# Performance work log

Hardware: AMD Instinct MI355X
Metric: run time of the kernel (lower is better)

Reference implementation:

```python
import jax, jax.numpy as jnp
import numpy as np

UFEAT_DIM = 256
MAPFEAT_DIM = 64


def setup_inputs() -> dict:
    key = jax.random.key(0)
    k1, k2, k3, k4 = jax.random.split(key, 4)
    ufeat = jax.random.normal(k1, (32, 512, UFEAT_DIM), dtype=jnp.float32)
    mapfeat = jax.random.normal(k2, (32, 4096, MAPFEAT_DIM), dtype=jnp.float32)
    # weight_norm(Linear, dim=None): W = g * V / ||V||_F, g scalar
    v_w = jax.random.normal(k3, (MAPFEAT_DIM, UFEAT_DIM), dtype=jnp.float32) * 0.05
    g = jnp.asarray(1.0, dtype=jnp.float32)
    b = jax.random.normal(k4, (MAPFEAT_DIM,), dtype=jnp.float32) * 0.05
    return {"ufeat": ufeat, "mapfeat": mapfeat, "v_w": v_w, "g": g, "b": b}


def reference(ufeat, mapfeat, v_w, g, b):
    # weight-normalized linear (dim=None -> scalar g over Frobenius norm)
    w = g * v_w / jnp.linalg.norm(v_w)
    proj = jax.nn.relu(jnp.einsum("bud,md->bum", ufeat, w) + b)  # [B, U, M]
    norm = jnp.sqrt(jnp.asarray(MAPFEAT_DIM, dtype=proj.dtype))
    # broadcast dot-product over spatial map, expressed as a batched matmul
    logit = jnp.einsum("bum,bsm->bus", proj, mapfeat) / norm  # [B, U, x*y]
    return logit
```

## Files before the change

kernel.cpp:

```cpp
#include <hip/hip_runtime.h>
#include <hip/hip_bf16.h>

typedef __bf16 bf16x8 __attribute__((ext_vector_type(8)));
typedef float  f32x16 __attribute__((ext_vector_type(16)));

#define UF_D 256
#define MAP_M 64
#define B_DIM 32
#define U_DIM 512
#define S_DIM 4096

__global__ __launch_bounds__(256) void prep_kernel(
    const float* __restrict__ v_w, const float* __restrict__ g,
    const float* __restrict__ b, __bf16* __restrict__ w_bf16,
    float* __restrict__ b_s)
{
    __shared__ float red[256];
    const int t = threadIdx.x;
    const float4* v4 = (const float4*)v_w;
    float ss = 0.f;
    for (int i = t; i < 4096; i += 256) {
        float4 v = v4[i];
        ss += v.x * v.x + v.y * v.y + v.z * v.z + v.w * v.w;
    }
    red[t] = ss;
    __syncthreads();
    for (int s = 128; s > 0; s >>= 1) {
        if (t < s) red[t] += red[t + s];
        __syncthreads();
    }
    const float scale = g[0] / (sqrtf(red[0]) * 8.0f);
    for (int i = t; i < 4096; i += 256) {
        float4 v = v4[i];
        w_bf16[4 * i + 0] = (__bf16)(v.x * scale);
        w_bf16[4 * i + 1] = (__bf16)(v.y * scale);
        w_bf16[4 * i + 2] = (__bf16)(v.z * scale);
        w_bf16[4 * i + 3] = (__bf16)(v.w * scale);
    }
    if (t < MAP_M) b_s[t] = b[t] * 0.125f;
}

__global__ __launch_bounds__(256) void proj_kernel(
    const float* __restrict__ ufeat,
    const __bf16* __restrict__ w,
    const float* __restrict__ b_s,
    __bf16* __restrict__ proj)
{
    const int wave = threadIdx.x >> 6;
    const int lane = threadIdx.x & 63;
    const int r = lane & 31;
    const int kh = lane >> 5;
    const int row0 = blockIdx.x * 128 + wave * 32;

    f32x16 acc0 = {};
    f32x16 acc1 = {};

    const float* arow = ufeat + (size_t)(row0 + r) * UF_D + kh * 8;
    const __bf16* b0p = w + r * UF_D + kh * 8;
    const __bf16* b1p = w + (32 + r) * UF_D + kh * 8;

#pragma unroll
    for (int k = 0; k < UF_D; k += 16) {
        float4 a01 = *(const float4*)(arow + k);
        float4 a23 = *(const float4*)(arow + k + 4);
        bf16x8 af;
        af[0] = (__bf16)a01.x; af[1] = (__bf16)a01.y;
        af[2] = (__bf16)a01.z; af[3] = (__bf16)a01.w;
        af[4] = (__bf16)a23.x; af[5] = (__bf16)a23.y;
        af[6] = (__bf16)a23.z; af[7] = (__bf16)a23.w;
        bf16x8 bf0 = *(const bf16x8*)(b0p + k);
        bf16x8 bf1 = *(const bf16x8*)(b1p + k);
        acc0 = __builtin_amdgcn_mfma_f32_32x32x16_bf16(af, bf0, acc0, 0, 0, 0);
        acc1 = __builtin_amdgcn_mfma_f32_32x32x16_bf16(af, bf1, acc1, 0, 0, 0);
    }

#pragma unroll
    for (int j = 0; j < 16; ++j) {
        const int rl = (j & 3) + 8 * (j >> 2) + 4 * kh;
        const size_t row = row0 + rl;
        float v0 = acc0[j] + b_s[r];
        float v1 = acc1[j] + b_s[32 + r];
        proj[row * MAP_M + r]      = (__bf16)fmaxf(v0, 0.f);
        proj[row * MAP_M + 32 + r] = (__bf16)fmaxf(v1, 0.f);
    }
}

__global__ __launch_bounds__(256) void logit_kernel(
    const __bf16* __restrict__ proj,
    const float* __restrict__ mapfeat,
    float* __restrict__ out)
{
    const int bid = blockIdx.x;
    const int ut = bid & 3;
    const int st = (bid >> 2) & 31;
    const int b  = bid >> 7;

    const int wave = threadIdx.x >> 6;
    const int lane = threadIdx.x & 63;
    const int wr = wave >> 1;
    const int wc = wave & 1;
    const int r  = lane & 31;
    const int kh = lane >> 5;

    const int u0 = ut * 128 + wr * 64;
    const int s0 = st * 128 + wc * 64;

    const __bf16* A = proj + (size_t)b * U_DIM * MAP_M;
    const float*  Bm = mapfeat + (size_t)b * S_DIM * MAP_M;

    f32x16 acc00 = {}, acc01 = {}, acc10 = {}, acc11 = {};

    const __bf16* a0p = A + (size_t)(u0 + r) * MAP_M + kh * 8;
    const __bf16* a1p = A + (size_t)(u0 + 32 + r) * MAP_M + kh * 8;
    const float*  b0p = Bm + (size_t)(s0 + r) * MAP_M + kh * 8;
    const float*  b1p = Bm + (size_t)(s0 + 32 + r) * MAP_M + kh * 8;

#pragma unroll
    for (int k = 0; k < MAP_M; k += 16) {
        bf16x8 a0 = *(const bf16x8*)(a0p + k);
        bf16x8 a1 = *(const bf16x8*)(a1p + k);
        float4 q0 = *(const float4*)(b0p + k);
        float4 q1 = *(const float4*)(b0p + k + 4);
        float4 q2 = *(const float4*)(b1p + k);
        float4 q3 = *(const float4*)(b1p + k + 4);
        bf16x8 bf0, bf1;
        bf0[0] = (__bf16)q0.x; bf0[1] = (__bf16)q0.y;
        bf0[2] = (__bf16)q0.z; bf0[3] = (__bf16)q0.w;
        bf0[4] = (__bf16)q1.x; bf0[5] = (__bf16)q1.y;
        bf0[6] = (__bf16)q1.z; bf0[7] = (__bf16)q1.w;
        bf1[0] = (__bf16)q2.x; bf1[1] = (__bf16)q2.y;
        bf1[2] = (__bf16)q2.z; bf1[3] = (__bf16)q2.w;
        bf1[4] = (__bf16)q3.x; bf1[5] = (__bf16)q3.y;
        bf1[6] = (__bf16)q3.z; bf1[7] = (__bf16)q3.w;
        acc00 = __builtin_amdgcn_mfma_f32_32x32x16_bf16(a0, bf0, acc00, 0, 0, 0);
        acc01 = __builtin_amdgcn_mfma_f32_32x32x16_bf16(a0, bf1, acc01, 0, 0, 0);
        acc10 = __builtin_amdgcn_mfma_f32_32x32x16_bf16(a1, bf0, acc10, 0, 0, 0);
        acc11 = __builtin_amdgcn_mfma_f32_32x32x16_bf16(a1, bf1, acc11, 0, 0, 0);
    }

    float* O = out + (size_t)b * U_DIM * S_DIM;
#pragma unroll
    for (int j = 0; j < 16; ++j) {
        const int rl = (j & 3) + 8 * (j >> 2) + 4 * kh;
        const size_t row0 = u0 + rl;
        const size_t row1 = u0 + 32 + rl;
        O[row0 * S_DIM + s0 + r]      = acc00[j];
        O[row0 * S_DIM + s0 + 32 + r] = acc01[j];
        O[row1 * S_DIM + s0 + r]      = acc10[j];
        O[row1 * S_DIM + s0 + 32 + r] = acc11[j];
    }
}

extern "C" void kernel_launch(void* const* d_in, const int* in_sizes, int n_in,
                              void* d_out, int out_size, void* d_ws, size_t ws_size,
                              hipStream_t stream) {
    const float* ufeat   = (const float*)d_in[0];
    const float* mapfeat = (const float*)d_in[1];
    const float* v_w     = (const float*)d_in[2];
    const float* g       = (const float*)d_in[3];
    const float* b       = (const float*)d_in[4];
    float* out = (float*)d_out;

    __bf16* w_bf16 = (__bf16*)d_ws;
    float*  b_s    = (float*)((char*)d_ws + 32768);
    __bf16* proj   = (__bf16*)((char*)d_ws + 65536);

    prep_kernel<<<1, 256, 0, stream>>>(v_w, g, b, w_bf16, b_s);
    proj_kernel<<<128, 256, 0, stream>>>(ufeat, w_bf16, b_s, proj);
    logit_kernel<<<B_DIM * 32 * 4, 256, 0, stream>>>(proj, mapfeat, out);
}
```

Before: 370.6 us.

## Pre-convert mapfeat to bf16, remap logit blocks, use nontemporal stores

Adds a pass in the prep kernel that converts mapfeat to bf16 once, using 255 extra blocks, so the logit kernel reads half-size bf16 tiles and no longer reconverts the same fp32 data for each of the 4 u-tiles. The logit block index is permuted so that blocks running at the same time spread across batches and tiles. Output stores and ufeat loads become nontemporal. proj_kernel is split into 256 blocks with one MFMA column tile per wave. The extra conversion pass costs an additional 32MB read and 16MB write of mapfeat.

```diff
diff --git a/kernel.cpp b/kernel.cpp
--- a/kernel.cpp
+++ b/kernel.cpp
@@ -3,6 +3,7 @@
 
 typedef __bf16 bf16x8 __attribute__((ext_vector_type(8)));
 typedef float  f32x16 __attribute__((ext_vector_type(16)));
+typedef float  f32x4  __attribute__((ext_vector_type(4)));
 
 #define UF_D 256
 #define MAP_M 64
@@ -10,34 +11,51 @@
 #define U_DIM 512
 #define S_DIM 4096
 
-__global__ __launch_bounds__(256) void prep_kernel(
+__global__ __launch_bounds__(256) void prep_conv_kernel(
     const float* __restrict__ v_w, const float* __restrict__ g,
-    const float* __restrict__ b, __bf16* __restrict__ w_bf16,
-    float* __restrict__ b_s)
+    const float* __restrict__ b, const float* __restrict__ mapfeat,
+    __bf16* __restrict__ w_bf16, float* __restrict__ b_s,
+    __bf16* __restrict__ map_bf16)
 {
-    __shared__ float red[256];
     const int t = threadIdx.x;
-    const float4* v4 = (const float4*)v_w;
-    float ss = 0.f;
-    for (int i = t; i < 4096; i += 256) {
-        float4 v = v4[i];
-        ss += v.x * v.x + v.y * v.y + v.z * v.z + v.w * v.w;
+    if (blockIdx.x == 0) {
+        __shared__ float red[256];
+        const f32x4* v4 = (const f32x4*)v_w;
+        float ss = 0.f;
+        for (int i = t; i < 4096; i += 256) {
+            f32x4 v = v4[i];
+            ss += v.x * v.x + v.y * v.y + v.z * v.z + v.w * v.w;
+        }
+        red[t] = ss;
+        __syncthreads();
+        for (int s = 128; s > 0; s >>= 1) {
+            if (t < s) red[t] += red[t + s];
+            __syncthreads();
+        }
+        const float scale = g[0] / (sqrtf(red[0]) * 8.0f);
+        for (int i = t; i < 4096; i += 256) {
+            f32x4 v = v4[i];
+            w_bf16[4 * i + 0] = (__bf16)(v.x * scale);
+            w_bf16[4 * i + 1] = (__bf16)(v.y * scale);
+            w_bf16[4 * i + 2] = (__bf16)(v.z * scale);
+            w_bf16[4 * i + 3] = (__bf16)(v.w * scale);
+        }
+        if (t < MAP_M) b_s[t] = b[t] * 0.125f;
+    } else {
+        const int NC = (B_DIM * S_DIM * MAP_M) / 8;
+        const f32x4* m4 = (const f32x4*)mapfeat;
+        bf16x8* o8 = (bf16x8*)map_bf16;
+        for (int c = (blockIdx.x - 1) * 256 + t; c < NC; c += 255 * 256) {
+            f32x4 q0 = __builtin_nontemporal_load(&m4[2 * c]);
+            f32x4 q1 = __builtin_nontemporal_load(&m4[2 * c + 1]);
+            bf16x8 o;
+            o[0] = (__bf16)q0.x; o[1] = (__bf16)q0.y;
+            o[2] = (__bf16)q0.z; o[3] = (__bf16)q0.w;
+            o[4] = (__bf16)q1.x; o[5] = (__bf16)q1.y;
+            o[6] = (__bf16)q1.z; o[7] = (__bf16)q1.w;
+            o8[c] = o;
+        }
     }
-    red[t] = ss;
-    __syncthreads();
-    for (int s = 128; s > 0; s >>= 1) {
-        if (t < s) red[t] += red[t + s];
-        __syncthreads();
-    }
-    const float scale = g[0] / (sqrtf(red[0]) * 8.0f);
-    for (int i = t; i < 4096; i += 256) {
-        float4 v = v4[i];
-        w_bf16[4 * i + 0] = (__bf16)(v.x * scale);
-        w_bf16[4 * i + 1] = (__bf16)(v.y * scale);
-        w_bf16[4 * i + 2] = (__bf16)(v.z * scale);
-        w_bf16[4 * i + 3] = (__bf16)(v.w * scale);
-    }
-    if (t < MAP_M) b_s[t] = b[t] * 0.125f;
 }
 
 __global__ __launch_bounds__(256) void proj_kernel(
@@ -48,94 +66,78 @@
 {
     const int wave = threadIdx.x >> 6;
     const int lane = threadIdx.x & 63;
-    const int r = lane & 31;
+    const int r  = lane & 31;
     const int kh = lane >> 5;
-    const int row0 = blockIdx.x * 128 + wave * 32;
+    const int wr = wave >> 1, wc = wave & 1;
+    const int row0 = blockIdx.x * 64 + wr * 32;
+    const int col0 = wc * 32;
 
-    f32x16 acc0 = {};
-    f32x16 acc1 = {};
-
-    const float* arow = ufeat + (size_t)(row0 + r) * UF_D + kh * 8;
-    const __bf16* b0p = w + r * UF_D + kh * 8;
-    const __bf16* b1p = w + (32 + r) * UF_D + kh * 8;
+    f32x16 acc = {};
+    const float*  ap = ufeat + (size_t)(row0 + r) * UF_D + kh * 8;
+    const __bf16* wp = w + (col0 + r) * UF_D + kh * 8;
 
 #pragma unroll
     for (int k = 0; k < UF_D; k += 16) {
-        float4 a01 = *(const float4*)(arow + k);
-        float4 a23 = *(const float4*)(arow + k + 4);
+        f32x4 a01 = __builtin_nontemporal_load((const f32x4*)(ap + k));
+        f32x4 a23 = __builtin_nontemporal_load((const f32x4*)(ap + k + 4));
         bf16x8 af;
         af[0] = (__bf16)a01.x; af[1] = (__bf16)a01.y;
         af[2] = (__bf16)a01.z; af[3] = (__bf16)a01.w;
         af[4] = (__bf16)a23.x; af[5] = (__bf16)a23.y;
         af[6] = (__bf16)a23.z; af[7] = (__bf16)a23.w;
-        bf16x8 bf0 = *(const bf16x8*)(b0p + k);
-        bf16x8 bf1 = *(const bf16x8*)(b1p + k);
-        acc0 = __builtin_amdgcn_mfma_f32_32x32x16_bf16(af, bf0, acc0, 0, 0, 0);
-        acc1 = __builtin_amdgcn_mfma_f32_32x32x16_bf16(af, bf1, acc1, 0, 0, 0);
+        bf16x8 wf = *(const bf16x8*)(wp + k);
+        acc = __builtin_amdgcn_mfma_f32_32x32x16_bf16(af, wf, acc, 0, 0, 0);
     }
 
 #pragma unroll
     for (int j = 0; j < 16; ++j) {
         const int rl = (j & 3) + 8 * (j >> 2) + 4 * kh;
         const size_t row = row0 + rl;
-        float v0 = acc0[j] + b_s[r];
-        float v1 = acc1[j] + b_s[32 + r];
-        proj[row * MAP_M + r]      = (__bf16)fmaxf(v0, 0.f);
-        proj[row * MAP_M + 32 + r] = (__bf16)fmaxf(v1, 0.f);
+        const int col = col0 + r;
+        float v = acc[j] + b_s[col];
+        proj[row * MAP_M + col] = (__bf16)fmaxf(v, 0.f);
     }
 }
 
 __global__ __launch_bounds__(256) void logit_kernel(
     const __bf16* __restrict__ proj,
-    const float* __restrict__ mapfeat,
+    const __bf16* __restrict__ map,
     float* __restrict__ out)
 {
-    const int bid = blockIdx.x;
-    const int ut = bid & 3;
-    const int st = (bid >> 2) & 31;
-    const int b  = bid >> 7;
+    const int vid = (blockIdx.x & 7) * 512 + (blockIdx.x >> 3);
+    const int ut = vid & 3;
+    const int st = (vid >> 2) & 31;
+    const int b  = vid >> 7;
 
     const int wave = threadIdx.x >> 6;
     const int lane = threadIdx.x & 63;
-    const int wr = wave >> 1;
-    const int wc = wave & 1;
+    const int wr = wave >> 1, wc = wave & 1;
     const int r  = lane & 31;
     const int kh = lane >> 5;
 
     const int u0 = ut * 128 + wr * 64;
     const int s0 = st * 128 + wc * 64;
 
-    const __bf16* A = proj + (size_t)b * U_DIM * MAP_M;
-    const float*  Bm = mapfeat + (size_t)b * S_DIM * MAP_M;
+    const __bf16* A  = proj + (size_t)b * U_DIM * MAP_M;
+    const __bf16* Bm = map  + (size_t)b * S_DIM * MAP_M;
 
     f32x16 acc00 = {}, acc01 = {}, acc10 = {}, acc11 = {};
 
-    const __bf16* a0p = A + (size_t)(u0 + r) * MAP_M + kh * 8;
-    const __bf16* a1p = A + (size_t)(u0 + 32 + r) * MAP_M + kh * 8;
-    const float*  b0p = Bm + (size_t)(s0 + r) * MAP_M + kh * 8;
-    const float*  b1p = Bm + (size_t)(s0 + 32 + r) * MAP_M + kh * 8;
+    const __bf16* a0p = A  + (size_t)(u0 + r)      * MAP_M + kh * 8;
+    const __bf16* a1p = A  + (size_t)(u0 + 32 + r) * MAP_M + kh * 8;
+    const __bf16* b0p = Bm + (size_t)(s0 + r)      * MAP_M + kh * 8;
+    const __bf16* b1p = Bm + (size_t)(s0 + 32 + r) * MAP_M + kh * 8;
 
 #pragma unroll
     for (int k = 0; k < MAP_M; k += 16) {
         bf16x8 a0 = *(const bf16x8*)(a0p + k);
         bf16x8 a1 = *(const bf16x8*)(a1p + k);
-        float4 q0 = *(const float4*)(b0p + k);
-        float4 q1 = *(const float4*)(b0p + k + 4);
-        float4 q2 = *(const float4*)(b1p + k);
-        float4 q3 = *(const float4*)(b1p + k + 4);
-        bf16x8 bf0, bf1;
-        bf0[0] = (__bf16)q0.x; bf0[1] = (__bf16)q0.y;
-        bf0[2] = (__bf16)q0.z; bf0[3] = (__bf16)q0.w;
-        bf0[4] = (__bf16)q1.x; bf0[5] = (__bf16)q1.y;
-        bf0[6] = (__bf16)q1.z; bf0[7] = (__bf16)q1.w;
-        bf1[0] = (__bf16)q2.x; bf1[1] = (__bf16)q2.y;
-        bf1[2] = (__bf16)q2.z; bf1[3] = (__bf16)q2.w;
-        bf1[4] = (__bf16)q3.x; bf1[5] = (__bf16)q3.y;
-        bf1[6] = (__bf16)q3.z; bf1[7] = (__bf16)q3.w;
-        acc00 = __builtin_amdgcn_mfma_f32_32x32x16_bf16(a0, bf0, acc00, 0, 0, 0);
-        acc01 = __builtin_amdgcn_mfma_f32_32x32x16_bf16(a0, bf1, acc01, 0, 0, 0);
-        acc10 = __builtin_amdgcn_mfma_f32_32x32x16_bf16(a1, bf0, acc10, 0, 0, 0);
-        acc11 = __builtin_amdgcn_mfma_f32_32x32x16_bf16(a1, bf1, acc11, 0, 0, 0);
+        bf16x8 f0 = *(const bf16x8*)(b0p + k);
+        bf16x8 f1 = *(const bf16x8*)(b1p + k);
+        acc00 = __builtin_amdgcn_mfma_f32_32x32x16_bf16(a0, f0, acc00, 0, 0, 0);
+        acc01 = __builtin_amdgcn_mfma_f32_32x32x16_bf16(a0, f1, acc01, 0, 0, 0);
+        acc10 = __builtin_amdgcn_mfma_f32_32x32x16_bf16(a1, f0, acc10, 0, 0, 0);
+        acc11 = __builtin_amdgcn_mfma_f32_32x32x16_bf16(a1, f1, acc11, 0, 0, 0);
     }
 
     float* O = out + (size_t)b * U_DIM * S_DIM;
@@ -144,10 +146,10 @@
         const int rl = (j & 3) + 8 * (j >> 2) + 4 * kh;
         const size_t row0 = u0 + rl;
         const size_t row1 = u0 + 32 + rl;
-        O[row0 * S_DIM + s0 + r]      = acc00[j];
-        O[row0 * S_DIM + s0 + 32 + r] = acc01[j];
-        O[row1 * S_DIM + s0 + r]      = acc10[j];
-        O[row1 * S_DIM + s0 + 32 + r] = acc11[j];
+        __builtin_nontemporal_store(acc00[j], &O[row0 * S_DIM + s0 + r]);
+        __builtin_nontemporal_store(acc01[j], &O[row0 * S_DIM + s0 + 32 + r]);
+        __builtin_nontemporal_store(acc10[j], &O[row1 * S_DIM + s0 + r]);
+        __builtin_nontemporal_store(acc11[j], &O[row1 * S_DIM + s0 + 32 + r]);
     }
 }
 
@@ -161,11 +163,12 @@
     const float* b       = (const float*)d_in[4];
     float* out = (float*)d_out;
 
-    __bf16* w_bf16 = (__bf16*)d_ws;
-    float*  b_s    = (float*)((char*)d_ws + 32768);
-    __bf16* proj   = (__bf16*)((char*)d_ws + 65536);
+    __bf16* w_bf16   = (__bf16*)d_ws;
+    float*  b_s      = (float*)((char*)d_ws + 32768);
+    __bf16* proj     = (__bf16*)((char*)d_ws + 65536);
+    __bf16* map_bf16 = (__bf16*)((char*)d_ws + 65536 + 2097152);
 
-    prep_kernel<<<1, 256, 0, stream>>>(v_w, g, b, w_bf16, b_s);
-    proj_kernel<<<128, 256, 0, stream>>>(ufeat, w_bf16, b_s, proj);
-    logit_kernel<<<B_DIM * 32 * 4, 256, 0, stream>>>(proj, mapfeat, out);
+    prep_conv_kernel<<<256, 256, 0, stream>>>(v_w, g, b, mapfeat, w_bf16, b_s, map_bf16);
+    proj_kernel<<<256, 256, 0, stream>>>(ufeat, w_bf16, b_s, proj);
+    logit_kernel<<<B_DIM * 32 * 4, 256, 0, stream>>>(proj, map_bf16, out);
 }
```

Result: faster. 328.5 us (-11.4%).
